# Kernel optimization log

Measured on AMD Instinct MI355X. Metric: run time of the kernel, lower is better.

The kernel has to match this reference:

```python
import jax, jax.numpy as jnp
import numpy as np

B, T, H = 8, 2048, 512


def _minimaxn(x):
    # global min-max normalization (NetTransform.minimaxn)
    mx = jnp.max(x)
    mn = jnp.min(x)
    return (x - mn) / (mx - mn)


def _fb(e):
    # NetTransform.fb, mode='batch', vectorized over the batch.
    # e: (B, 1, T) -> (B, 1, T, T)
    # Result: out[b,0,i,j] = prod(e[b,0,j:i]) for i>j, 1 on diag, 0 above diag.
    x = e[:, 0]                                   # (B, T)
    Bsz, Tsz = x.shape
    X = jnp.broadcast_to(x[:, :, None], (Bsz, Tsz, Tsz))  # xs = x.unsqueeze(-1).repeat(1,1,T)
    tril1 = jnp.tril(jnp.ones((Tsz, Tsz), x.dtype))
    m_f = jnp.triu(jnp.ones((Tsz, Tsz), x.dtype), 1)
    A = X * tril1 + m_f                           # tril(x) + m_f
    C = jnp.cumprod(A, axis=1)                    # cumprod along dim -2
    S = jnp.concatenate([jnp.ones((Bsz, 1, Tsz), x.dtype), C[:, :-1]], axis=1) - m_f
    return S[:, None]                             # (B, 1, T, T)


def _clustering(energy_t):
    # NetTransform.clustering (tnum == 1), vectorized over batch.
    # energy_t: (B, 1, T) -> bool mask (B, 1, T) with top-num_neg of (1-energy) set True
    x = 1.0 - energy_t[:, 0]                      # (B, T)
    num_neg = x.sum(-1).astype(jnp.int32)         # int() truncation; x >= 0 so == floor
    ranks = jnp.argsort(jnp.argsort(-x, axis=-1), axis=-1)  # rank 0 = largest
    m = ranks < num_neg[:, None]
    return m[:, None]                             # (B, 1, T)


def setup_inputs() -> dict:
    key = jax.random.key(0)
    k1, k2, k3 = jax.random.split(key, 3)
    e = jax.random.uniform(k1, (B, 1, T), dtype=jnp.float32)
    h = jax.random.normal(k2, (B, 1, T, H), dtype=jnp.float32)
    ilens = jnp.concatenate([
        jnp.array([T], dtype=jnp.int32),
        jax.random.randint(k3, (B - 1,), T // 2, T + 1).astype(jnp.int32),
    ])
    return {"e": e, "h": h, "ilens": ilens}


def reference(e, h, ilens):
    sg = jax.lax.stop_gradient
    # energy_t = minimaxn(flows['e']).detach()
    energy_t = sg(_minimaxn(e))                   # (B, 1, T)
    # clustering mask (computed in forward; unused when cutting_gauge == 0)
    _ = _clustering(energy_t)
    # energy_t_cumprod = fb(energy_t)  (under no_grad)
    K = sg(_fb(energy_t))                         # (B, 1, T, T)
    # h_agg = (K @ h) / K.sum(-1, keepdim), then transpose(-2, -1)
    h_agg = jnp.einsum('bnts,bnsh->bnth', K, h) / K.sum(-1, keepdims=True)
    h_agg = jnp.swapaxes(h_agg, -2, -1)           # (B, 1, H, T)
    # kernel = (h @ h_agg.detach() + h.detach() @ h_agg) / 2 / sqrt(H)
    kernel = (jnp.matmul(h, sg(h_agg)) + jnp.matmul(sg(h), h_agg)) / 2.0 / np.sqrt(H).astype(np.float32)
    return kernel                                 # (B, 1, T, T)
```

## Files before the change

### kernel.cpp

```cpp
#include <hip/hip_runtime.h>
#include <hip/hip_bf16.h>
#include <stdint.h>

#define B_DIM 8
#define T_DIM 2048
#define H_DIM 512
#define NC 32
#define LCH 64
#define NSUB 4
#define LSUB 16
#define NSEG (NC * NSUB)
#define NOCT 8
#define BM 128
#define BN 128
#define BK 64

typedef float floatx4 __attribute__((ext_vector_type(4)));
typedef __bf16 bf16x4 __attribute__((ext_vector_type(4)));
typedef __bf16 bf16x8 __attribute__((ext_vector_type(8)));

__device__ __forceinline__ void block_minmax(const float* __restrict__ e,
                                             float* __restrict__ sst ,
                                             float* __restrict__ smn ,
                                             float* __restrict__ smx ) {
    const int tid = threadIdx.x;
    const float4* e4 = (const float4*)e;
    float mn = 1e30f, mx = -1e30f;
    #pragma unroll
    for (int i = 0; i < 8; ++i) {
        float4 v = e4[tid + i * 512];
        mn = fminf(mn, fminf(fminf(v.x, v.y), fminf(v.z, v.w)));
        mx = fmaxf(mx, fmaxf(fmaxf(v.x, v.y), fmaxf(v.z, v.w)));
    }
    #pragma unroll
    for (int off = 32; off > 0; off >>= 1) {
        mn = fminf(mn, __shfl_down(mn, off, 64));
        mx = fmaxf(mx, __shfl_down(mx, off, 64));
    }
    const int wid = tid >> 6;
    if ((tid & 63) == 0) { smn[wid] = mn; smx[wid] = mx; }
    __syncthreads();
    if (tid == 0) {
        mn = smn[0]; mx = smx[0];
        #pragma unroll
        for (int w = 1; w < 8; ++w) { mn = fminf(mn, smn[w]); mx = fmaxf(mx, smx[w]); }
        sst[0] = mn;
        sst[1] = 1.0f / (mx - mn);
    }
    __syncthreads();
}

__global__ __launch_bounds__(512) void chunk_sum_kernel(
        const float* __restrict__ e, const float* __restrict__ h,
        __hip_bfloat16* __restrict__ h_bf,
        float* __restrict__ Lsub, float* __restrict__ PPsub, float* __restrict__ LDsub) {
    const int b = blockIdx.x, c = blockIdx.y;
    const int tid = threadIdx.x;
    const int hdq = tid & 127, sub = tid >> 7;
    const int hd = hdq * 4;
    const int t0 = c * LCH + sub * LSUB;

    __shared__ float sst[2], smn[8], smx[8];
    __shared__ float se[LCH];
    block_minmax(e, sst, smn, smx);

    if (tid < LCH) {
        int t = c * LCH + tid;
        se[tid] = (t == 0) ? 0.0f : (e[b * T_DIM + t - 1] - sst[0]) * sst[1];
    }
    __syncthreads();

    const float* hp = h + ((size_t)b * T_DIM + t0) * H_DIM + hd;
    __hip_bfloat16* hbp = h_bf + ((size_t)b * T_DIM + t0) * H_DIM + hd;

    floatx4 lv = {0.0f, 0.0f, 0.0f, 0.0f};
    float ldv = 0.0f, pp = 1.0f;
    #pragma unroll 8
    for (int i = 0; i < LSUB; ++i) {
        float a = se[sub * LSUB + i];
        floatx4 hv = *(const floatx4*)(hp + (size_t)i * H_DIM);
        lv = a * lv + hv;
        ldv = fmaf(a, ldv, 1.0f);
        pp *= a;
        bf16x4 o;
        #pragma unroll
        for (int k = 0; k < 4; ++k) o[k] = (__bf16)hv[k];
        *(bf16x4*)(hbp + (size_t)i * H_DIM) = o;
    }
    int seg = (b * NC + c) * NSUB + sub;
    *(floatx4*)(Lsub + (size_t)seg * H_DIM + hd) = lv;
    if (hdq == 0) { PPsub[seg] = pp; LDsub[seg] = ldv; }
}

__global__ __launch_bounds__(512) void octprefix_kernel(
        const float* __restrict__ Lsub, const float* __restrict__ PPsub,
        const float* __restrict__ LDsub,
        float* __restrict__ Spart, float* __restrict__ Ppre, float* __restrict__ SDpart,
        float* __restrict__ Loct, float* __restrict__ Poct, float* __restrict__ LDoct) {
    const int b = blockIdx.x, o = blockIdx.y, hd = threadIdx.x;
    float sp = 0.0f, sdp = 0.0f, pp = 1.0f;
    #pragma unroll 4
    for (int i = 0; i < 16; ++i) {
        int seg = b * NSEG + o * 16 + i;
        Spart[(size_t)seg * H_DIM + hd] = sp;
        if (hd == 0) { Ppre[seg] = pp; SDpart[seg] = sdp; }
        float pe = PPsub[seg];
        sp  = fmaf(pe, sp,  Lsub[(size_t)seg * H_DIM + hd]);
        sdp = fmaf(pe, sdp, LDsub[seg]);
        pp *= pe;
    }
    int oc = b * NOCT + o;
    Loct[(size_t)oc * H_DIM + hd] = sp;
    if (hd == 0) { Poct[oc] = pp; LDoct[oc] = sdp; }
}

__global__ __launch_bounds__(512) void octfold_kernel(
        const float* __restrict__ Loct, const float* __restrict__ Poct,
        const float* __restrict__ LDoct,
        float* __restrict__ Soct, float* __restrict__ SDoct) {
    const int b = blockIdx.x, hd = threadIdx.x;
    float s = 0.0f, sd = 0.0f;
    #pragma unroll
    for (int o = 0; o < NOCT; ++o) {
        int oc = b * NOCT + o;
        Soct[(size_t)oc * H_DIM + hd] = s;
        if (hd == 0) SDoct[oc] = sd;
        float P = Poct[oc];
        s  = fmaf(P, s,  Loct[(size_t)oc * H_DIM + hd]);
        sd = fmaf(P, sd, LDoct[oc]);
    }
}

__global__ __launch_bounds__(512) void rescan_kernel(
        const float* __restrict__ e, const __hip_bfloat16* __restrict__ h_bf,
        const float* __restrict__ Spart, const float* __restrict__ Ppre,
        const float* __restrict__ SDpart,
        const float* __restrict__ Soct, const float* __restrict__ SDoct,
        __hip_bfloat16* __restrict__ hagg_bf) {
    const int b = blockIdx.x, c = blockIdx.y;
    const int tid = threadIdx.x;
    const int hdq = tid & 127, sub = tid >> 7;
    const int hd = hdq * 4;
    const int t0 = c * LCH + sub * LSUB;

    __shared__ float sst[2], smn[8], smx[8];
    __shared__ float se[LCH];
    block_minmax(e, sst, smn, smx);

    if (tid < LCH) {
        int t = c * LCH + tid;
        se[tid] = (t == 0) ? 0.0f : (e[b * T_DIM + t - 1] - sst[0]) * sst[1];
    }
    __syncthreads();

    const int seg = (b * NC + c) * NSUB + sub;
    const int oc  = b * NOCT + (c >> 2);
    const __hip_bfloat16* hbp = h_bf + ((size_t)b * T_DIM + t0) * H_DIM + hd;
    __hip_bfloat16* hop = hagg_bf + ((size_t)b * T_DIM + t0) * H_DIM + hd;

    const float pq = Ppre[seg];
    floatx4 soct  = *(const floatx4*)(Soct  + (size_t)oc  * H_DIM + hd);
    floatx4 spart = *(const floatx4*)(Spart + (size_t)seg * H_DIM + hd);
    floatx4 s = pq * soct + spart;
    float sd = fmaf(pq, SDoct[oc], SDpart[seg]);

    #pragma unroll 8
    for (int i = 0; i < LSUB; ++i) {
        float a = se[sub * LSUB + i];
        bf16x4 hb = *(const bf16x4*)(hbp + (size_t)i * H_DIM);
        floatx4 hv;
        #pragma unroll
        for (int k = 0; k < 4; ++k) hv[k] = (float)hb[k];
        s = a * s + hv;
        sd = fmaf(a, sd, 1.0f);
        float inv = 1.0f / sd;
        bf16x4 o;
        #pragma unroll
        for (int k = 0; k < 4; ++k) o[k] = (__bf16)(s[k] * inv);
        *(bf16x4*)(hop + (size_t)i * H_DIM) = o;
    }
}

__device__ __forceinline__ void async16(const void* g, void* l) {
    __builtin_amdgcn_global_load_lds(
        (__attribute__((address_space(1))) void*)g,
        (__attribute__((address_space(3))) void*)l,
        16, 0, 0);
}

__global__ __launch_bounds__(256) void gemm_kernel(
        const __hip_bfloat16* __restrict__ Abf,
        const __hip_bfloat16* __restrict__ Bbf,
        float* __restrict__ C) {
    __shared__ __align__(16) __hip_bfloat16 As[BM * BK];
    __shared__ __align__(16) __hip_bfloat16 Bs[BN * BK];

    const int id = blockIdx.x + (blockIdx.y << 4) + (blockIdx.z << 8);
    const int b  = id & 7;
    const int tt = id >> 3;
    const int tm = (tt & 15) * BM;
    const int sn = (tt >> 4) * BN;

    const int tid = threadIdx.x;
    const int lane = tid & 63;
    const int wave = tid >> 6;
    const int wm = (wave >> 1) * 64;
    const int wn = (wave & 1) * 64;
    const int l16 = lane & 15;
    const int quad = lane >> 4;

    const int srow = tid >> 3;
    const int sgran = (tid & 7) ^ (srow & 7);
    const __hip_bfloat16* Ag = Abf + ((size_t)b * T_DIM + tm + srow) * H_DIM + sgran * 8;
    const __hip_bfloat16* Bg = Bbf + ((size_t)b * T_DIM + sn + srow) * H_DIM + sgran * 8;
    char* AsB = (char*)As;
    char* BsB = (char*)Bs;

    floatx4 zero = {0.0f, 0.0f, 0.0f, 0.0f};
    floatx4 acc[4][4];
    #pragma unroll
    for (int i = 0; i < 4; ++i)
        #pragma unroll
        for (int j = 0; j < 4; ++j) acc[i][j] = zero;

    for (int kk = 0; kk < H_DIM; kk += BK) {
        __syncthreads();
        #pragma unroll
        for (int q = 0; q < 4; ++q) {
            async16(Ag + (size_t)q * 32 * H_DIM + kk, AsB + q * 4096 + tid * 16);
            async16(Bg + (size_t)q * 32 * H_DIM + kk, BsB + q * 4096 + tid * 16);
        }
        asm volatile("s_waitcnt vmcnt(0)" ::: "memory");
        __syncthreads();

        bf16x8 af[2][4], bfv[2][4];
        #pragma unroll
        for (int ku = 0; ku < 2; ++ku)
            #pragma unroll
            for (int i = 0; i < 4; ++i) {
                int ra = wm + i * 16 + l16;
                int rb = wn + i * 16 + l16;
                int ga = (ku * 4 + quad) ^ (l16 & 7);
                af[ku][i]  = *reinterpret_cast<const bf16x8*>(AsB + ra * 128 + ga * 16);
                bfv[ku][i] = *reinterpret_cast<const bf16x8*>(BsB + rb * 128 + ga * 16);
            }
        #pragma unroll
        for (int ku = 0; ku < 2; ++ku)
            #pragma unroll
            for (int i = 0; i < 4; ++i)
                #pragma unroll
                for (int j = 0; j < 4; ++j)
                    acc[i][j] = __builtin_amdgcn_mfma_f32_16x16x32_bf16(bfv[ku][j], af[ku][i], acc[i][j], 0, 0, 0);
    }

    const float scale = 0.04419417382415922f;
    float* Cp = C + (size_t)b * T_DIM * T_DIM;
    #pragma unroll
    for (int i = 0; i < 4; ++i) {
        int row = tm + wm + i * 16 + l16;
        float* crow = Cp + (size_t)row * T_DIM;
        #pragma unroll
        for (int j = 0; j < 4; ++j) {
            int col = sn + wn + j * 16 + quad * 4;
            floatx4 v;
            #pragma unroll
            for (int r = 0; r < 4; ++r) v[r] = acc[i][j][r] * scale;
            *(floatx4*)(crow + col) = v;
        }
    }
}

extern "C" void kernel_launch(void* const* d_in, const int* in_sizes, int n_in,
                              void* d_out, int out_size, void* d_ws, size_t ws_size,
                              hipStream_t stream) {
    const float* e = (const float*)d_in[0];
    const float* h = (const float*)d_in[1];
    float* out = (float*)d_out;

    char* ws = (char*)d_ws;
    __hip_bfloat16* h_bf    = (__hip_bfloat16*)(ws + 4096);
    __hip_bfloat16* hagg_bf = (__hip_bfloat16*)(ws + 4096 + (16u << 20));
    char* p = ws + 4096 + (32u << 20);
    float* Lsub  = (float*)p;   p += (size_t)B_DIM * NSEG * H_DIM * 4;
    float* Spart = (float*)p;   p += (size_t)B_DIM * NSEG * H_DIM * 4;
    float* PPsub = (float*)p;   p += B_DIM * NSEG * 4;
    float* LDsub = (float*)p;   p += B_DIM * NSEG * 4;
    float* Ppre  = (float*)p;   p += B_DIM * NSEG * 4;
    float* SDpart= (float*)p;   p += B_DIM * NSEG * 4;
    float* Loct  = (float*)p;   p += (size_t)B_DIM * NOCT * H_DIM * 4;
    float* Soct  = (float*)p;   p += (size_t)B_DIM * NOCT * H_DIM * 4;
    float* Poct  = (float*)p;   p += B_DIM * NOCT * 4;
    float* LDoct = (float*)p;   p += B_DIM * NOCT * 4;
    float* SDoct = (float*)p;

    chunk_sum_kernel<<<dim3(B_DIM, NC), 512, 0, stream>>>(e, h, h_bf, Lsub, PPsub, LDsub);
    octprefix_kernel<<<dim3(B_DIM, NOCT), 512, 0, stream>>>(Lsub, PPsub, LDsub,
                                                            Spart, Ppre, SDpart,
                                                            Loct, Poct, LDoct);
    octfold_kernel<<<B_DIM, 512, 0, stream>>>(Loct, Poct, LDoct, Soct, SDoct);
    rescan_kernel<<<dim3(B_DIM, NC), 512, 0, stream>>>(e, h_bf, Spart, Ppre, SDpart,
                                                       Soct, SDoct, hagg_bf);
    gemm_kernel<<<dim3(T_DIM / BM, T_DIM / BN, B_DIM), 256, 0, stream>>>(h_bf, hagg_bf, out);
}
```

Before: 208.1 us.

## Double-buffer GEMM K-loop with BK=32 and fold octave prefix into rescan

The GEMM now loads the next K tile into a second LDS buffer while MFMAs run on the current one. It uses BK=32 with a matching XOR swizzle, s_setprio around the MFMA block, and partial vmcnt waits, so global-to-LDS latency can overlap with compute. Separately, the octfold kernel is removed: each rescan block recomputes its octave prefix from Loct/Poct/LDoct, which saves one launch and one global round trip. The cost is more barriers per K element and a small amount of redundant prefix work in each rescan block.

```diff
diff --git a/kernel.cpp b/kernel.cpp
--- a/kernel.cpp
+++ b/kernel.cpp
@@ -13,7 +13,7 @@
 #define NOCT 8
 #define BM 128
 #define BN 128
-#define BK 64
+#define BK 32
 
 typedef float floatx4 __attribute__((ext_vector_type(4)));
 typedef __bf16 bf16x4 __attribute__((ext_vector_type(4)));
@@ -114,28 +114,12 @@
     if (hd == 0) { Poct[oc] = pp; LDoct[oc] = sdp; }
 }
 
-__global__ __launch_bounds__(512) void octfold_kernel(
-        const float* __restrict__ Loct, const float* __restrict__ Poct,
-        const float* __restrict__ LDoct,
-        float* __restrict__ Soct, float* __restrict__ SDoct) {
-    const int b = blockIdx.x, hd = threadIdx.x;
-    float s = 0.0f, sd = 0.0f;
-    #pragma unroll
-    for (int o = 0; o < NOCT; ++o) {
-        int oc = b * NOCT + o;
-        Soct[(size_t)oc * H_DIM + hd] = s;
-        if (hd == 0) SDoct[oc] = sd;
-        float P = Poct[oc];
-        s  = fmaf(P, s,  Loct[(size_t)oc * H_DIM + hd]);
-        sd = fmaf(P, sd, LDoct[oc]);
-    }
-}
-
 __global__ __launch_bounds__(512) void rescan_kernel(
         const float* __restrict__ e, const __hip_bfloat16* __restrict__ h_bf,
         const float* __restrict__ Spart, const float* __restrict__ Ppre,
         const float* __restrict__ SDpart,
-        const float* __restrict__ Soct, const float* __restrict__ SDoct,
+        const float* __restrict__ Loct, const float* __restrict__ Poct,
+        const float* __restrict__ LDoct,
         __hip_bfloat16* __restrict__ hagg_bf) {
     const int b = blockIdx.x, c = blockIdx.y;
     const int tid = threadIdx.x;
@@ -154,15 +138,24 @@
     __syncthreads();
 
     const int seg = (b * NC + c) * NSUB + sub;
-    const int oc  = b * NOCT + (c >> 2);
+    const int oct = c >> 2;
     const __hip_bfloat16* hbp = h_bf + ((size_t)b * T_DIM + t0) * H_DIM + hd;
     __hip_bfloat16* hop = hagg_bf + ((size_t)b * T_DIM + t0) * H_DIM + hd;
 
+    floatx4 soct = {0.0f, 0.0f, 0.0f, 0.0f};
+    float sdoct = 0.0f;
+    for (int o = 0; o < oct; ++o) {
+        int oc = b * NOCT + o;
+        float P = Poct[oc];
+        floatx4 lo = *(const floatx4*)(Loct + (size_t)oc * H_DIM + hd);
+        soct = P * soct + lo;
+        sdoct = fmaf(P, sdoct, LDoct[oc]);
+    }
+
     const float pq = Ppre[seg];
-    floatx4 soct  = *(const floatx4*)(Soct  + (size_t)oc  * H_DIM + hd);
     floatx4 spart = *(const floatx4*)(Spart + (size_t)seg * H_DIM + hd);
     floatx4 s = pq * soct + spart;
-    float sd = fmaf(pq, SDoct[oc], SDpart[seg]);
+    float sd = fmaf(pq, sdoct, SDpart[seg]);
 
     #pragma unroll 8
     for (int i = 0; i < LSUB; ++i) {
@@ -192,8 +185,9 @@
         const __hip_bfloat16* __restrict__ Abf,
         const __hip_bfloat16* __restrict__ Bbf,
         float* __restrict__ C) {
-    __shared__ __align__(16) __hip_bfloat16 As[BM * BK];
-    __shared__ __align__(16) __hip_bfloat16 Bs[BN * BK];
+    __shared__ __align__(16) char lds[32768];
+    char* AsB = lds;
+    char* BsB = lds + 16384;
 
     const int id = blockIdx.x + (blockIdx.y << 4) + (blockIdx.z << 8);
     const int b  = id & 7;
@@ -209,12 +203,10 @@
     const int l16 = lane & 15;
     const int quad = lane >> 4;
 
-    const int srow = tid >> 3;
-    const int sgran = (tid & 7) ^ (srow & 7);
-    const __hip_bfloat16* Ag = Abf + ((size_t)b * T_DIM + tm + srow) * H_DIM + sgran * 8;
-    const __hip_bfloat16* Bg = Bbf + ((size_t)b * T_DIM + sn + srow) * H_DIM + sgran * 8;
-    char* AsB = (char*)As;
-    char* BsB = (char*)Bs;
+    const int srow = tid >> 2;
+    const int sg = (tid & 3) ^ ((srow >> 1) & 3);
+    const __hip_bfloat16* Ag = Abf + ((size_t)b * T_DIM + tm + srow) * H_DIM + sg * 8;
+    const __hip_bfloat16* Bg = Bbf + ((size_t)b * T_DIM + sn + srow) * H_DIM + sg * 8;
 
     floatx4 zero = {0.0f, 0.0f, 0.0f, 0.0f};
     floatx4 acc[4][4];
@@ -223,35 +215,53 @@
         #pragma unroll
         for (int j = 0; j < 4; ++j) acc[i][j] = zero;
 
-    for (int kk = 0; kk < H_DIM; kk += BK) {
-        __syncthreads();
-        #pragma unroll
-        for (int q = 0; q < 4; ++q) {
-            async16(Ag + (size_t)q * 32 * H_DIM + kk, AsB + q * 4096 + tid * 16);
-            async16(Bg + (size_t)q * 32 * H_DIM + kk, BsB + q * 4096 + tid * 16);
+    #define STAGE(kt, buf) do {                                                   \
+        const int kk_ = (kt) * BK;                                                \
+        async16(Ag + kk_,                        AsB + (buf) * 8192 + tid * 16);  \
+        async16(Ag + (size_t)64 * H_DIM + kk_,   AsB + (buf) * 8192 + 4096 + tid * 16); \
+        async16(Bg + kk_,                        BsB + (buf) * 8192 + tid * 16);  \
+        async16(Bg + (size_t)64 * H_DIM + kk_,   BsB + (buf) * 8192 + 4096 + tid * 16); \
+    } while (0)
+
+    STAGE(0, 0);
+    const int NT = H_DIM / BK;
+    for (int t = 0; t < NT; ++t) {
+        const int cur = t & 1;
+        if (t < NT - 1) {
+            STAGE(t + 1, cur ^ 1);
+            asm volatile("s_waitcnt vmcnt(4)" ::: "memory");
+        } else {
+            asm volatile("s_waitcnt vmcnt(0)" ::: "memory");
         }
-        asm volatile("s_waitcnt vmcnt(0)" ::: "memory");
-        __syncthreads();
-
-        bf16x8 af[2][4], bfv[2][4];
-        #pragma unroll
-        for (int ku = 0; ku < 2; ++ku)
+        __builtin_amdgcn_s_barrier();
+
+        const char* Ab = AsB + cur * 8192;
+        const char* Bb = BsB + cur * 8192;
+        bf16x8 af[4], bv[4];
+        #pragma unroll
+        for (int j = 0; j < 4; ++j) {
+            int rb = wn + j * 16 + l16;
+            int gb = quad ^ ((rb >> 1) & 3);
+            bv[j] = *reinterpret_cast<const bf16x8*>(Bb + rb * 64 + gb * 16);
+        }
+        #pragma unroll
+        for (int i = 0; i < 4; ++i) {
+            int ra = wm + i * 16 + l16;
+            int ga = quad ^ ((ra >> 1) & 3);
+            af[i] = *reinterpret_cast<const bf16x8*>(Ab + ra * 64 + ga * 16);
+        }
+        __builtin_amdgcn_s_setprio(1);
+        #pragma unroll
+        for (int i = 0; i < 4; ++i)
             #pragma unroll
-            for (int i = 0; i < 4; ++i) {
-                int ra = wm + i * 16 + l16;
-                int rb = wn + i * 16 + l16;
-                int ga = (ku * 4 + quad) ^ (l16 & 7);
-                af[ku][i]  = *reinterpret_cast<const bf16x8*>(AsB + ra * 128 + ga * 16);
-                bfv[ku][i] = *reinterpret_cast<const bf16x8*>(BsB + rb * 128 + ga * 16);
-            }
-        #pragma unroll
-        for (int ku = 0; ku < 2; ++ku)
-            #pragma unroll
-            for (int i = 0; i < 4; ++i)
-                #pragma unroll
-                for (int j = 0; j < 4; ++j)
-                    acc[i][j] = __builtin_amdgcn_mfma_f32_16x16x32_bf16(bfv[ku][j], af[ku][i], acc[i][j], 0, 0, 0);
-    }
+            for (int j = 0; j < 4; ++j)
+                acc[i][j] = __builtin_amdgcn_mfma_f32_16x16x32_bf16(
+                    bv[j], af[i], acc[i][j], 0, 0, 0);
+        __builtin_amdgcn_s_setprio(0);
+        asm volatile("s_waitcnt lgkmcnt(0)" ::: "memory");
+        __builtin_amdgcn_s_barrier();
+    }
+    #undef STAGE
 
     const float scale = 0.04419417382415922f;
     float* Cp = C + (size_t)b * T_DIM * T_DIM;
@@ -288,17 +298,14 @@
     float* Ppre  = (float*)p;   p += B_DIM * NSEG * 4;
     float* SDpart= (float*)p;   p += B_DIM * NSEG * 4;
     float* Loct  = (float*)p;   p += (size_t)B_DIM * NOCT * H_DIM * 4;
-    float* Soct  = (float*)p;   p += (size_t)B_DIM * NOCT * H_DIM * 4;
     float* Poct  = (float*)p;   p += B_DIM * NOCT * 4;
-    float* LDoct = (float*)p;   p += B_DIM * NOCT * 4;
-    float* SDoct = (float*)p;
+    float* LDoct = (float*)p;
 
     chunk_sum_kernel<<<dim3(B_DIM, NC), 512, 0, stream>>>(e, h, h_bf, Lsub, PPsub, LDsub);
     octprefix_kernel<<<dim3(B_DIM, NOCT), 512, 0, stream>>>(Lsub, PPsub, LDsub,
                                                             Spart, Ppre, SDpart,
                                                             Loct, Poct, LDoct);
-    octfold_kernel<<<B_DIM, 512, 0, stream>>>(Loct, Poct, LDoct, Soct, SDoct);
     rescan_kernel<<<dim3(B_DIM, NC), 512, 0, stream>>>(e, h_bf, Spart, Ppre, SDpart,
-                                                       Soct, SDoct, hagg_bf);
+                                                       Loct, Poct, LDoct, hagg_bf);
     gemm_kernel<<<dim3(T_DIM / BM, T_DIM / BN, B_DIM), 256, 0, stream>>>(h_bf, hagg_bf, out);
 }
```

Measured after the change: 209.9 us. No clear change (+0.9%).
